# Optimization experiments

Measured on AMD Instinct MI355X. Metric: run time of the kernel, lower is better.

The kernel has to match this reference:

```python
import jax, jax.numpy as jnp
import numpy as np

N_HIDDEN_LAYERS = 9  # 32->32 middle layers (plus input 1->32 and output 32->1)
HID = 32
SLOPE = 0.01  # LeakyReLU negative_slope


def leaky_relu(x):
    return jnp.where(x >= 0, x, SLOPE * x)


def setup_inputs() -> dict:
    key = jax.random.key(0)
    ks = jax.random.split(key, 8)
    N = 1048576
    x = jax.random.normal(ks[0], (N,), dtype=jnp.float32)
    # PyTorch Linear init: U(-1/sqrt(fan_in), 1/sqrt(fan_in))
    def u(k, shape, fan_in):
        b = 1.0 / np.sqrt(fan_in)
        return jax.random.uniform(k, shape, jnp.float32, -b, b)
    W_in = u(ks[1], (1, HID), 1)
    b_in = u(ks[2], (HID,), 1)
    W_hid = u(ks[3], (N_HIDDEN_LAYERS, HID, HID), HID)
    b_hid = u(ks[4], (N_HIDDEN_LAYERS, HID), HID)
    W_out = u(ks[5], (HID, 1), HID)
    b_out = u(ks[6], (1,), HID)
    return {"x": x, "W_in": W_in, "b_in": b_in, "W_hid": W_hid,
            "b_hid": b_hid, "W_out": W_out, "b_out": b_out}


def reference(x, W_in, b_in, W_hid, b_hid, W_out, b_out):
    N = x.shape[0]
    h = x[:, None]  # [N, 1], mirrors x.reshape(N, 1)
    h = leaky_relu(h @ W_in + b_in)  # [N, 32]
    def step(h, wb):
        W, b = wb
        return leaky_relu(h @ W + b), None
    h, _ = jax.lax.scan(step, h, (W_hid, b_hid))
    out = h @ W_out + b_out  # [N, 1]
    return out.reshape(1, N)
```

## Files before the change

kernel.cpp:

```cpp
#include <hip/hip_runtime.h>

#define NLAYERS 9
#define HID 32
#define SLOPE 0.01f

typedef _Float16 v2h __attribute__((ext_vector_type(2)));
typedef _Float16 v8h __attribute__((ext_vector_type(8)));
typedef float v16f __attribute__((ext_vector_type(16)));

#define NCHAIN 4

union U8 { v8h v; v2h p[4]; };

__device__ __forceinline__ v2h pk_cvt(float a, float b) {
    return __builtin_bit_cast(v2h, __builtin_amdgcn_cvt_pkrtz(a, b));
}
__device__ __forceinline__ v2h leaky2(v2h t, v2h s) {
    return __builtin_elementwise_max(t, t * s);
}
__device__ __forceinline__ int qmap(int k) {
    int c = k >> 4, h = (k >> 3) & 1, t = k & 7;
    return 16 * c + 4 * h + (t & 3) + 8 * (t >> 2);
}
__device__ __forceinline__ int rmap(int reg, int h) {
    return (reg & 3) + 8 * (reg >> 2) + 4 * h;
}

__global__ __launch_bounds__(256, 3) void mlp_mfma_kernel(
    const float* __restrict__ x,
    const float* __restrict__ W_in,
    const float* __restrict__ b_in,
    const float* __restrict__ W_hid,
    const float* __restrict__ b_hid,
    const float* __restrict__ W_out,
    const float* __restrict__ b_out,
    float* __restrict__ out, int N)
{
    __shared__ __align__(16) _Float16 wlo_sh[NLAYERS][64][8];
    __shared__ __align__(16) _Float16 whi_sh[NLAYERS][64][8];
    __shared__ __align__(64) float bc_sh[NLAYERS][2][16];

    const int tid = threadIdx.x;
    for (int t = tid; t < NLAYERS * 64; t += blockDim.x) {
        int l = t >> 6, ln = t & 63, hf = (ln >> 5) & 1, mm = ln & 31;
        const float* Wl = W_hid + l * HID * HID;
        v8h lo, hi;
#pragma unroll
        for (int j = 0; j < 8; ++j) {
            lo[j] = (_Float16)Wl[qmap(8 * hf + j) * HID + mm];
            hi[j] = (_Float16)Wl[qmap(16 + 8 * hf + j) * HID + mm];
        }
        *(v8h*)&wlo_sh[l][ln][0] = lo;
        *(v8h*)&whi_sh[l][ln][0] = hi;
    }
    for (int t = tid; t < NLAYERS * 32; t += blockDim.x) {
        int l = t >> 5, r = t & 31, hf = r >> 4, reg = r & 15;
        bc_sh[l][hf][reg] = b_hid[l * HID + rmap(reg, hf)];
    }
    __syncthreads();

    const int lane = tid & 63;
    const int half = lane >> 5;
    const int m    = lane & 31;

    v2h win2[8], bin2[8], wout2[8];
#pragma unroll
    for (int u = 0; u < 8; ++u) {
        int i0 = 2 * u, i1 = 2 * u + 1;
        int d0 = qmap(((i0 >> 3) << 4) + 8 * half + (i0 & 7));
        int d1 = qmap(((i1 >> 3) << 4) + 8 * half + (i1 & 7));
        win2[u]  = v2h{(_Float16)W_in[d0],  (_Float16)W_in[d1]};
        bin2[u]  = v2h{(_Float16)b_in[d0],  (_Float16)b_in[d1]};
        wout2[u] = v2h{(_Float16)W_out[d0], (_Float16)W_out[d1]};
    }
    const float bo = b_out[0];
    const v2h slope2 = v2h{(_Float16)SLOPE, (_Float16)SLOPE};

    const int nwaves = (gridDim.x * blockDim.x) >> 6;
    const int wid    = (blockIdx.x * blockDim.x + tid) >> 6;
    const int niter  = (N + NCHAIN * 32 - 1) / (NCHAIN * 32);

    float xc[NCHAIN] = {0.0f, 0.0f, 0.0f, 0.0f};
    if (wid < niter) {
#pragma unroll
        for (int c = 0; c < NCHAIN; ++c) {
            int idx = wid * (NCHAIN * 32) + c * 32 + m;
            xc[c] = (idx < N) ? x[idx] : 0.0f;
        }
    }

    for (int it = wid; it < niter; it += nwaves) {
        float xn[NCHAIN] = {0.0f, 0.0f, 0.0f, 0.0f};
        {
            int nit = it + nwaves;
            if (nit < niter) {
#pragma unroll
                for (int c = 0; c < NCHAIN; ++c) {
                    int idx = nit * (NCHAIN * 32) + c * 32 + m;
                    xn[c] = (idx < N) ? x[idx] : 0.0f;
                }
            }
        }

        U8 clo[NCHAIN], chi[NCHAIN];
#pragma unroll
        for (int c = 0; c < NCHAIN; ++c) {
            _Float16 xh = (_Float16)xc[c];
            v2h x2 = v2h{xh, xh};
#pragma unroll
            for (int u = 0; u < 4; ++u) {
                clo[c].p[u] = leaky2(x2 * win2[u] + bin2[u], slope2);
                chi[c].p[u] = leaky2(x2 * win2[4 + u] + bin2[4 + u], slope2);
            }
        }

#pragma unroll 1
        for (int l = 0; l < NLAYERS; ++l) {
            v8h wlo = *(const v8h*)&wlo_sh[l][lane][0];
            v8h whi = *(const v8h*)&whi_sh[l][lane][0];
            v16f bc = *(const v16f*)&bc_sh[l][half][0];
#pragma unroll
            for (int g = 0; g < NCHAIN / 2; ++g) {
                const int c0 = 2 * g, c1 = 2 * g + 1;
                v16f a0 = __builtin_amdgcn_mfma_f32_32x32x16_f16(wlo, clo[c0].v, bc, 0, 0, 0);
                v16f a1 = __builtin_amdgcn_mfma_f32_32x32x16_f16(wlo, clo[c1].v, bc, 0, 0, 0);
                a0 = __builtin_amdgcn_mfma_f32_32x32x16_f16(whi, chi[c0].v, a0, 0, 0, 0);
                a1 = __builtin_amdgcn_mfma_f32_32x32x16_f16(whi, chi[c1].v, a1, 0, 0, 0);
#pragma unroll
                for (int u = 0; u < 4; ++u) {
                    clo[c0].p[u] = leaky2(pk_cvt(a0[2 * u], a0[2 * u + 1]), slope2);
                    chi[c0].p[u] = leaky2(pk_cvt(a0[8 + 2 * u], a0[8 + 2 * u + 1]), slope2);
                    clo[c1].p[u] = leaky2(pk_cvt(a1[2 * u], a1[2 * u + 1]), slope2);
                    chi[c1].p[u] = leaky2(pk_cvt(a1[8 + 2 * u], a1[8 + 2 * u + 1]), slope2);
                }
            }
        }

#pragma unroll
        for (int c = 0; c < NCHAIN; ++c) {
            float p = 0.0f;
#pragma unroll
            for (int u = 0; u < 4; ++u) {
                p = fmaf((float)clo[c].p[u][0], (float)wout2[u][0], p);
                p = fmaf((float)clo[c].p[u][1], (float)wout2[u][1], p);
                p = fmaf((float)chi[c].p[u][0], (float)wout2[4 + u][0], p);
                p = fmaf((float)chi[c].p[u][1], (float)wout2[4 + u][1], p);
            }
            float o = p + __shfl_xor(p, 32, 64) + bo;
            int idx = it * (NCHAIN * 32) + c * 32 + m;
            if (half == (c >> 1) && idx < N) out[idx] = o;
        }

#pragma unroll
        for (int c = 0; c < NCHAIN; ++c) xc[c] = xn[c];
    }
}

extern "C" void kernel_launch(void* const* d_in, const int* in_sizes, int n_in,
                              void* d_out, int out_size, void* d_ws, size_t ws_size,
                              hipStream_t stream) {
    const float* x     = (const float*)d_in[0];
    const float* W_in  = (const float*)d_in[1];
    const float* b_in  = (const float*)d_in[2];
    const float* W_hid = (const float*)d_in[3];
    const float* b_hid = (const float*)d_in[4];
    const float* W_out = (const float*)d_in[5];
    const float* b_out = (const float*)d_in[6];
    float* out = (float*)d_out;

    int N = in_sizes[0];
    dim3 block(256);
    dim3 grid(768);
    mlp_mfma_kernel<<<grid, block, 0, stream>>>(x, W_in, b_in, W_hid, b_hid,
                                                W_out, b_out, out, N);
}
```

Baseline: 89.92 us.

## Switch hidden layers from 32x32x16 to 16x16x32 MFMA tiling

Replaces the 32x32x16 f16 MFMA chain per layer with 16x16x32 MFMAs. The 32 outputs are split into two 16-row tiles and the 32 samples of each chain into two 16-column halves, with weights re-laid-out in shared memory so an MFMA's output registers feed straight into the next layer's B operand. It also prefetches the next layer's weights and bias from LDS one iteration ahead, and uses fdot2 for the output projection. The aim is to shorten MFMA dependency latency and raise instruction-level parallelism, at the cost of twice as many MFMA issues and more cross-lane shuffles in the output reduction.

Measured after the change: 92.67 us. +3.1%, slower.

```diff
diff --git a/kernel.cpp b/kernel.cpp
--- a/kernel.cpp
+++ b/kernel.cpp
@@ -6,7 +6,7 @@
 
 typedef _Float16 v2h __attribute__((ext_vector_type(2)));
 typedef _Float16 v8h __attribute__((ext_vector_type(8)));
-typedef float v16f __attribute__((ext_vector_type(16)));
+typedef float v4f __attribute__((ext_vector_type(4)));
 
 #define NCHAIN 4
 
@@ -18,12 +18,8 @@
 __device__ __forceinline__ v2h leaky2(v2h t, v2h s) {
     return __builtin_elementwise_max(t, t * s);
 }
-__device__ __forceinline__ int qmap(int k) {
-    int c = k >> 4, h = (k >> 3) & 1, t = k & 7;
-    return 16 * c + 4 * h + (t & 3) + 8 * (t >> 2);
-}
-__device__ __forceinline__ int rmap(int reg, int h) {
-    return (reg & 3) + 8 * (reg >> 2) + 4 * h;
+__device__ __forceinline__ int umap(int g, int j) {
+    return 4 * g + (j & 3) + 16 * (j >> 2);
 }
 
 __global__ __launch_bounds__(256, 3) void mlp_mfma_kernel(
@@ -36,42 +32,35 @@
     const float* __restrict__ b_out,
     float* __restrict__ out, int N)
 {
-    __shared__ __align__(16) _Float16 wlo_sh[NLAYERS][64][8];
-    __shared__ __align__(16) _Float16 whi_sh[NLAYERS][64][8];
+    __shared__ __align__(16) _Float16 wA_sh[NLAYERS][2][64][8];
     __shared__ __align__(64) float bc_sh[NLAYERS][2][16];
 
     const int tid = threadIdx.x;
-    for (int t = tid; t < NLAYERS * 64; t += blockDim.x) {
-        int l = t >> 6, ln = t & 63, hf = (ln >> 5) & 1, mm = ln & 31;
+    for (int t = tid; t < NLAYERS * 2 * 64; t += blockDim.x) {
+        int l = t >> 7, r = t & 127, tt = (r >> 6) & 1, ln = r & 63;
+        int i = ln & 15, g = ln >> 4;
         const float* Wl = W_hid + l * HID * HID;
-        v8h lo, hi;
+        v8h w;
 #pragma unroll
-        for (int j = 0; j < 8; ++j) {
-            lo[j] = (_Float16)Wl[qmap(8 * hf + j) * HID + mm];
-            hi[j] = (_Float16)Wl[qmap(16 + 8 * hf + j) * HID + mm];
-        }
-        *(v8h*)&wlo_sh[l][ln][0] = lo;
-        *(v8h*)&whi_sh[l][ln][0] = hi;
+        for (int j = 0; j < 8; ++j)
+            w[j] = (_Float16)Wl[umap(g, j) * HID + 16 * tt + i];
+        *(v8h*)&wA_sh[l][tt][ln][0] = w;
     }
-    for (int t = tid; t < NLAYERS * 32; t += blockDim.x) {
-        int l = t >> 5, r = t & 31, hf = r >> 4, reg = r & 15;
-        bc_sh[l][hf][reg] = b_hid[l * HID + rmap(reg, hf)];
-    }
+    for (int t = tid; t < NLAYERS * HID; t += blockDim.x)
+        ((float*)bc_sh)[t] = b_hid[t];
     __syncthreads();
 
     const int lane = tid & 63;
-    const int half = lane >> 5;
-    const int m    = lane & 31;
+    const int g    = lane >> 4;
+    const int col  = lane & 15;
 
-    v2h win2[8], bin2[8], wout2[8];
+    v2h win2[4], bin2[4], wout2[4];
 #pragma unroll
-    for (int u = 0; u < 8; ++u) {
-        int i0 = 2 * u, i1 = 2 * u + 1;
-        int d0 = qmap(((i0 >> 3) << 4) + 8 * half + (i0 & 7));
-        int d1 = qmap(((i1 >> 3) << 4) + 8 * half + (i1 & 7));
-        win2[u]  = v2h{(_Float16)W_in[d0],  (_Float16)W_in[d1]};
-        bin2[u]  = v2h{(_Float16)b_in[d0],  (_Float16)b_in[d1]};
-        wout2[u] = v2h{(_Float16)W_out[d0], (_Float16)W_out[d1]};
+    for (int jj = 0; jj < 4; ++jj) {
+        int u0 = umap(g, 2 * jj), u1 = umap(g, 2 * jj + 1);
+        win2[jj]  = v2h{(_Float16)W_in[u0],  (_Float16)W_in[u1]};
+        bin2[jj]  = v2h{(_Float16)b_in[u0],  (_Float16)b_in[u1]};
+        wout2[jj] = v2h{(_Float16)W_out[u0], (_Float16)W_out[u1]};
     }
     const float bo = b_out[0];
     const v2h slope2 = v2h{(_Float16)SLOPE, (_Float16)SLOPE};
@@ -80,79 +69,103 @@
     const int wid    = (blockIdx.x * blockDim.x + tid) >> 6;
     const int niter  = (N + NCHAIN * 32 - 1) / (NCHAIN * 32);
 
-    float xc[NCHAIN] = {0.0f, 0.0f, 0.0f, 0.0f};
+    float xc[2 * NCHAIN] = {};
     if (wid < niter) {
 #pragma unroll
-        for (int c = 0; c < NCHAIN; ++c) {
-            int idx = wid * (NCHAIN * 32) + c * 32 + m;
-            xc[c] = (idx < N) ? x[idx] : 0.0f;
-        }
+        for (int c = 0; c < NCHAIN; ++c)
+#pragma unroll
+            for (int nh = 0; nh < 2; ++nh) {
+                int idx = wid * (NCHAIN * 32) + c * 32 + 16 * nh + col;
+                xc[2 * c + nh] = (idx < N) ? x[idx] : 0.0f;
+            }
     }
 
     for (int it = wid; it < niter; it += nwaves) {
-        float xn[NCHAIN] = {0.0f, 0.0f, 0.0f, 0.0f};
+        float xn[2 * NCHAIN] = {};
         {
             int nit = it + nwaves;
             if (nit < niter) {
 #pragma unroll
-                for (int c = 0; c < NCHAIN; ++c) {
-                    int idx = nit * (NCHAIN * 32) + c * 32 + m;
-                    xn[c] = (idx < N) ? x[idx] : 0.0f;
-                }
+                for (int c = 0; c < NCHAIN; ++c)
+#pragma unroll
+                    for (int nh = 0; nh < 2; ++nh) {
+                        int idx = nit * (NCHAIN * 32) + c * 32 + 16 * nh + col;
+                        xn[2 * c + nh] = (idx < N) ? x[idx] : 0.0f;
+                    }
             }
         }
 
-        U8 clo[NCHAIN], chi[NCHAIN];
+        U8 f[NCHAIN][2];
 #pragma unroll
-        for (int c = 0; c < NCHAIN; ++c) {
-            _Float16 xh = (_Float16)xc[c];
-            v2h x2 = v2h{xh, xh};
+        for (int c = 0; c < NCHAIN; ++c)
 #pragma unroll
-            for (int u = 0; u < 4; ++u) {
-                clo[c].p[u] = leaky2(x2 * win2[u] + bin2[u], slope2);
-                chi[c].p[u] = leaky2(x2 * win2[4 + u] + bin2[4 + u], slope2);
+            for (int nh = 0; nh < 2; ++nh) {
+                _Float16 xh = (_Float16)xc[2 * c + nh];
+                v2h x2 = v2h{xh, xh};
+#pragma unroll
+                for (int jj = 0; jj < 4; ++jj)
+                    f[c][nh].p[jj] = leaky2(x2 * win2[jj] + bin2[jj], slope2);
             }
-        }
 
+        v8h wA0 = *(const v8h*)&wA_sh[0][0][lane][0];
+        v8h wA1 = *(const v8h*)&wA_sh[0][1][lane][0];
+        v4f bc0 = *(const v4f*)&bc_sh[0][0][4 * g];
+        v4f bc1 = *(const v4f*)&bc_sh[0][1][4 * g];
 #pragma unroll 1
         for (int l = 0; l < NLAYERS; ++l) {
-            v8h wlo = *(const v8h*)&wlo_sh[l][lane][0];
-            v8h whi = *(const v8h*)&whi_sh[l][lane][0];
-            v16f bc = *(const v16f*)&bc_sh[l][half][0];
+            const int lnx = (l + 1 < NLAYERS) ? l + 1 : l;
+            v8h wA0n = *(const v8h*)&wA_sh[lnx][0][lane][0];
+            v8h wA1n = *(const v8h*)&wA_sh[lnx][1][lane][0];
+            v4f bc0n = *(const v4f*)&bc_sh[lnx][0][4 * g];
+            v4f bc1n = *(const v4f*)&bc_sh[lnx][1][4 * g];
 #pragma unroll
-            for (int g = 0; g < NCHAIN / 2; ++g) {
-                const int c0 = 2 * g, c1 = 2 * g + 1;
-                v16f a0 = __builtin_amdgcn_mfma_f32_32x32x16_f16(wlo, clo[c0].v, bc, 0, 0, 0);
-                v16f a1 = __builtin_amdgcn_mfma_f32_32x32x16_f16(wlo, clo[c1].v, bc, 0, 0, 0);
-                a0 = __builtin_amdgcn_mfma_f32_32x32x16_f16(whi, chi[c0].v, a0, 0, 0, 0);
-                a1 = __builtin_amdgcn_mfma_f32_32x32x16_f16(whi, chi[c1].v, a1, 0, 0, 0);
-#pragma unroll
-                for (int u = 0; u < 4; ++u) {
-                    clo[c0].p[u] = leaky2(pk_cvt(a0[2 * u], a0[2 * u + 1]), slope2);
-                    chi[c0].p[u] = leaky2(pk_cvt(a0[8 + 2 * u], a0[8 + 2 * u + 1]), slope2);
-                    clo[c1].p[u] = leaky2(pk_cvt(a1[2 * u], a1[2 * u + 1]), slope2);
-                    chi[c1].p[u] = leaky2(pk_cvt(a1[8 + 2 * u], a1[8 + 2 * u + 1]), slope2);
-                }
+            for (int gr = 0; gr < NCHAIN / 2; ++gr) {
+                const int c0 = 2 * gr, c1 = 2 * gr + 1;
+                v4f a0t0h0 = __builtin_amdgcn_mfma_f32_16x16x32_f16(wA0, f[c0][0].v, bc0, 0, 0, 0);
+                v4f a0t0h1 = __builtin_amdgcn_mfma_f32_16x16x32_f16(wA0, f[c0][1].v, bc0, 0, 0, 0);
+                v4f a0t1h0 = __builtin_amdgcn_mfma_f32_16x16x32_f16(wA1, f[c0][0].v, bc1, 0, 0, 0);
+                v4f a0t1h1 = __builtin_amdgcn_mfma_f32_16x16x32_f16(wA1, f[c0][1].v, bc1, 0, 0, 0);
+                v4f a1t0h0 = __builtin_amdgcn_mfma_f32_16x16x32_f16(wA0, f[c1][0].v, bc0, 0, 0, 0);
+                v4f a1t0h1 = __builtin_amdgcn_mfma_f32_16x16x32_f16(wA0, f[c1][1].v, bc0, 0, 0, 0);
+                v4f a1t1h0 = __builtin_amdgcn_mfma_f32_16x16x32_f16(wA1, f[c1][0].v, bc1, 0, 0, 0);
+                v4f a1t1h1 = __builtin_amdgcn_mfma_f32_16x16x32_f16(wA1, f[c1][1].v, bc1, 0, 0, 0);
+                f[c0][0].p[0] = leaky2(pk_cvt(a0t0h0[0], a0t0h0[1]), slope2);
+                f[c0][0].p[1] = leaky2(pk_cvt(a0t0h0[2], a0t0h0[3]), slope2);
+                f[c0][0].p[2] = leaky2(pk_cvt(a0t1h0[0], a0t1h0[1]), slope2);
+                f[c0][0].p[3] = leaky2(pk_cvt(a0t1h0[2], a0t1h0[3]), slope2);
+                f[c0][1].p[0] = leaky2(pk_cvt(a0t0h1[0], a0t0h1[1]), slope2);
+                f[c0][1].p[1] = leaky2(pk_cvt(a0t0h1[2], a0t0h1[3]), slope2);
+                f[c0][1].p[2] = leaky2(pk_cvt(a0t1h1[0], a0t1h1[1]), slope2);
+                f[c0][1].p[3] = leaky2(pk_cvt(a0t1h1[2], a0t1h1[3]), slope2);
+                f[c1][0].p[0] = leaky2(pk_cvt(a1t0h0[0], a1t0h0[1]), slope2);
+                f[c1][0].p[1] = leaky2(pk_cvt(a1t0h0[2], a1t0h0[3]), slope2);
+                f[c1][0].p[2] = leaky2(pk_cvt(a1t1h0[0], a1t1h0[1]), slope2);
+                f[c1][0].p[3] = leaky2(pk_cvt(a1t1h0[2], a1t1h0[3]), slope2);
+                f[c1][1].p[0] = leaky2(pk_cvt(a1t0h1[0], a1t0h1[1]), slope2);
+                f[c1][1].p[1] = leaky2(pk_cvt(a1t0h1[2], a1t0h1[3]), slope2);
+                f[c1][1].p[2] = leaky2(pk_cvt(a1t1h1[0], a1t1h1[1]), slope2);
+                f[c1][1].p[3] = leaky2(pk_cvt(a1t1h1[2], a1t1h1[3]), slope2);
             }
+            wA0 = wA0n; wA1 = wA1n; bc0 = bc0n; bc1 = bc1n;
         }
 
 #pragma unroll
-        for (int c = 0; c < NCHAIN; ++c) {
-            float p = 0.0f;
+        for (int c = 0; c < NCHAIN; ++c)
 #pragma unroll
-            for (int u = 0; u < 4; ++u) {
-                p = fmaf((float)clo[c].p[u][0], (float)wout2[u][0], p);
-                p = fmaf((float)clo[c].p[u][1], (float)wout2[u][1], p);
-                p = fmaf((float)chi[c].p[u][0], (float)wout2[4 + u][0], p);
-                p = fmaf((float)chi[c].p[u][1], (float)wout2[4 + u][1], p);
+            for (int nh = 0; nh < 2; ++nh) {
+                float p = 0.0f;
+#pragma unroll
+                for (int jj = 0; jj < 4; ++jj)
+                    p = __builtin_amdgcn_fdot2(f[c][nh].p[jj], wout2[jj], p, false);
+                p += __shfl_xor(p, 16, 64);
+                p += __shfl_xor(p, 32, 64);
+                float o = p + bo;
+                int idx = it * (NCHAIN * 32) + c * 32 + 16 * nh + col;
+                if (g == 2 * (c & 1) + nh && idx < N) out[idx] = o;
             }
-            float o = p + __shfl_xor(p, 32, 64) + bo;
-            int idx = it * (NCHAIN * 32) + c * 32 + m;
-            if (half == (c >> 1) && idx < N) out[idx] = o;
-        }
 
 #pragma unroll
-        for (int c = 0; c < NCHAIN; ++c) xc[c] = xn[c];
+        for (int q = 0; q < 2 * NCHAIN; ++q) xc[q] = xn[q];
     }
 }
 
```
